# Optimization experiments

Measured on AMD Instinct MI355X. Metric: run time of the kernel, lower is better.

The kernel has to match this reference:

```python
import jax, jax.numpy as jnp
import numpy as np

SIZES = jnp.array([128.0, 256.0, 512.0], dtype=jnp.float32)
RATIOS = jnp.array([0.5, 1.0, 2.0], dtype=jnp.float32)
SCORE_THR = 0.05
IOU_THR = 0.7
MIN_SIZE = 16.0
MAX_PROP = 1000
PRE_NMS = 1000


def _base_anchors():
    # torchvision-style base anchors: (x1,y1,x2,y2) centered at origin, rounded
    h_r = jnp.sqrt(RATIOS)
    w_r = 1.0 / h_r
    ws = (w_r[:, None] * SIZES[None, :]).reshape(-1)  # (9,)
    hs = (h_r[:, None] * SIZES[None, :]).reshape(-1)
    return jnp.round(jnp.stack([-ws, -hs, ws, hs], axis=1) / 2.0)  # (9,4)


def _grid_anchors(img_h, img_w, fh, fw):
    # stride = image_size // feature_size; anchors ordered (y, x, anchor)
    sh, sw = img_h // fh, img_w // fw
    sx = jnp.arange(fw, dtype=jnp.float32) * sw
    sy = jnp.arange(fh, dtype=jnp.float32) * sh
    yy, xx = jnp.meshgrid(sy, sx, indexing='ij')
    xf = xx.reshape(-1)
    yf = yy.reshape(-1)
    shifts = jnp.stack([xf, yf, xf, yf], axis=1)  # (H*W, 4)
    return (shifts[:, None, :] + _base_anchors()[None, :, :]).reshape(-1, 4)  # (H*W*9, 4)


def _conv(x, w, b, pad):
    y = jax.lax.conv_general_dilated(x, w, (1, 1), pad,
                                     dimension_numbers=('NCHW', 'OIHW', 'NCHW'))
    return y + b[None, :, None, None]


def _bbox_adjust(anchors, deltas):
    # anchors, deltas: (..., 4); deltas = (dx, dy, dw, dh)
    aw = anchors[..., 2] - anchors[..., 0]
    ah = anchors[..., 3] - anchors[..., 1]
    cx = anchors[..., 0] + 0.5 * aw
    cy = anchors[..., 1] + 0.5 * ah
    ncx = deltas[..., 0] * aw + cx
    ncy = deltas[..., 1] * ah + cy
    nw = jnp.exp(deltas[..., 2]) * aw
    nh = jnp.exp(deltas[..., 3]) * ah
    return jnp.stack([ncx - 0.5 * nw, ncy - 0.5 * nh,
                      ncx + 0.5 * nw, ncy + 0.5 * nh], axis=-1)


def _pairwise_iou(b):
    area = (b[:, 2] - b[:, 0]) * (b[:, 3] - b[:, 1])
    lt = jnp.maximum(b[:, None, :2], b[None, :, :2])
    rb = jnp.minimum(b[:, None, 2:], b[None, :, 2:])
    wh = jnp.clip(rb - lt, 0.0)
    inter = wh[..., 0] * wh[..., 1]
    return inter / (area[:, None] + area[None, :] - inter + 1e-8)


def _per_image(boxes, scores, img_h, img_w):
    # clip to image, filter small / low-score, greedy NMS, pad to MAX_PROP
    x1 = jnp.clip(boxes[:, 0], 0.0, img_w)
    y1 = jnp.clip(boxes[:, 1], 0.0, img_h)
    x2 = jnp.clip(boxes[:, 2], 0.0, img_w)
    y2 = jnp.clip(boxes[:, 3], 0.0, img_h)
    b = jnp.stack([x1, y1, x2, y2], axis=1)
    valid = ((x2 - x1) >= MIN_SIZE) & ((y2 - y1) >= MIN_SIZE) & (scores > SCORE_THR)
    s = jnp.where(valid, scores, -1.0)
    topv, topi = jax.lax.top_k(s, PRE_NMS)
    tb = b[topi]  # (PRE_NMS, 4) sorted by score desc
    iou = _pairwise_iou(tb)
    idx = jnp.arange(PRE_NMS)

    def body(i, keep):
        sup = (iou[i] > IOU_THR) & keep[i] & (idx > i)
        return keep & ~sup

    keep = jax.lax.fori_loop(0, PRE_NMS, body, jnp.ones(PRE_NMS, dtype=bool))
    s2 = jnp.where(keep & (topv > 0.0), topv, -1.0)
    fv, fi = jax.lax.top_k(s2, MAX_PROP)
    return jnp.where((fv > 0.0)[:, None], tb[fi], 0.0)  # (MAX_PROP, 4)


def _forward(image_list, feature_map, conv_w, conv_b, cls_w, cls_b, bbox_w, bbox_b):
    N, C, H, W = feature_map.shape
    img_h, img_w = image_list.shape[2], image_list.shape[3]
    out = _conv(feature_map, conv_w, conv_b, 'SAME')  # (N, mid, H, W)
    # faithful to original: cls reshaped directly (no permute), bbox permuted
    cls = jax.nn.sigmoid(_conv(out, cls_w, cls_b, 'VALID')).reshape(N, -1, 2)
    bb = _conv(out, bbox_w, bbox_b, 'VALID').transpose(0, 2, 3, 1).reshape(N, -1, 4)
    anchors = _grid_anchors(img_h, img_w, H, W)  # (H*W*9, 4)
    dec = _bbox_adjust(anchors[None], bb)        # (N, M, 4)
    scores = cls[:, :, 1]                        # objectness
    fh, fw = float(img_h), float(img_w)
    fb = jax.vmap(lambda bx, sc: _per_image(bx, sc, fh, fw))(dec, scores)  # (N, MAX_PROP, 4)
    roi = fb.reshape(-1, 4)
    bidx = jnp.repeat(jnp.arange(N, dtype=roi.dtype), MAX_PROP)[:, None]
    return jnp.concatenate([roi, bidx], axis=1)  # (N*MAX_PROP, 5)


def setup_inputs() -> dict:
    key = jax.random.key(0)
    ks = jax.random.split(key, 6)
    image_list = jax.random.normal(ks[0], (8, 3, 800, 800), dtype=jnp.float32)
    feature_map = jax.random.normal(ks[1], (8, 512, 50, 50), dtype=jnp.float32)
    conv_w = 0.02 * jax.random.normal(ks[2], (256, 512, 3, 3), dtype=jnp.float32)
    conv_b = jnp.zeros((256,), dtype=jnp.float32)
    cls_w = 0.02 * jax.random.normal(ks[3], (18, 256, 1, 1), dtype=jnp.float32)
    cls_b = jnp.zeros((18,), dtype=jnp.float32)
    bbox_w = 0.01 * jax.random.normal(ks[4], (36, 256, 1, 1), dtype=jnp.float32)
    bbox_b = jnp.zeros((36,), dtype=jnp.float32)
    return {"image_list": image_list, "feature_map": feature_map,
            "conv_w": conv_w, "conv_b": conv_b, "cls_w": cls_w, "cls_b": cls_b,
            "bbox_w": bbox_w, "bbox_b": bbox_b}


def reference(image_list, feature_map, conv_w, conv_b, cls_w, cls_b, bbox_w, bbox_b):
    return _forward(image_list, feature_map, conv_w, conv_b, cls_w, cls_b, bbox_w, bbox_b)
```

## Files before the change

### kernel.cpp

```cpp
#include <hip/hip_runtime.h>
#include <cstdint>

#define N_IMG 8
#define CIN 512
#define COUT 256
#define FH 50
#define FW 50
#define SPAT 2500
#define NANCH 22500
#define KTOP 1000

__global__ __launch_bounds__(128) void k_conv3(const float* __restrict__ in,
                                               const float* __restrict__ w,
                                               const float* __restrict__ bias,
                                               float* __restrict__ out)
{
    __shared__ double ind[2][672];

    const int tile = blockIdx.x, ocg = blockIdx.y, n = blockIdx.z;
    const int ty = tile / 5, tx = tile % 5;
    const int y0 = ty * 5, x0 = tx * 10;
    const int t = threadIdx.x;
    const int oc_l = t & 63;
    const int g = t >> 6;
    const int base_lx = g * 5;
    const int oc0 = ocg * 64;

    int soff[6];
#pragma unroll
    for (int k = 0; k < 6; k++) {
        int idx = t + k * 128;
        soff[k] = -1;
        if (idx < 672) {
            int c = idx / 84, rem = idx - c * 84;
            int iy = rem / 12, ix = rem - iy * 12;
            int y = y0 - 1 + iy, x = x0 - 1 + ix;
            if ((unsigned)y < 50u && (unsigned)x < 50u)
                soff[k] = (n * CIN + c) * SPAT + y * FW + x;
        }
    }

    const float* wrow = w + (size_t)(oc0 + oc_l) * (CIN * 9);

    double acc[5][5];
#pragma unroll
    for (int i = 0; i < 5; i++)
#pragma unroll
        for (int j = 0; j < 5; j++) acc[i][j] = 0.0;

    float rin[6];
#pragma unroll
    for (int k = 0; k < 6; k++) rin[k] = (soff[k] >= 0) ? in[soff[k]] : 0.0f;
    float wnxt[9];
#pragma unroll
    for (int k = 0; k < 9; k++) wnxt[k] = wrow[k];

    for (int cc = 0; cc < 64; ++cc) {
        const int cur = cc & 1;
#pragma unroll
        for (int k = 0; k < 6; k++) {
            int idx = t + k * 128;
            if (idx < 672) ind[cur][idx] = (double)rin[k];
        }
        __syncthreads();

        if (cc < 63) {
            const int coff = (cc + 1) * (8 * SPAT);
#pragma unroll
            for (int k = 0; k < 6; k++)
                rin[k] = (soff[k] >= 0) ? in[soff[k] + coff] : 0.0f;
        }

#pragma unroll 1
        for (int c = 0; c < 8; c++) {
            double wd[9];
#pragma unroll
            for (int k = 0; k < 9; k++) wd[k] = (double)wnxt[k];
            const int nidx = cc * 8 + c + 1;
            if (nidx < 512) {
                const float* wp = wrow + nidx * 9;
#pragma unroll
                for (int k = 0; k < 9; k++) wnxt[k] = wp[k];
            }
#pragma unroll
            for (int r = 0; r < 7; r++) {
                double drow[7];
#pragma unroll
                for (int j = 0; j < 7; j++)
                    drow[j] = ind[cur][c * 84 + r * 12 + base_lx + j];
#pragma unroll
                for (int dy = 0; dy < 3; dy++) {
                    const int iy = r - dy;
                    if (iy >= 0 && iy < 5) {
#pragma unroll
                        for (int dx = 0; dx < 3; dx++) {
                            const double wdv = wd[dy * 3 + dx];
#pragma unroll
                            for (int ix = 0; ix < 5; ix++)
                                acc[iy][ix] = fma(wdv, drow[ix + dx], acc[iy][ix]);
                        }
                    }
                }
            }
        }
    }

    const double b = (double)bias[oc0 + oc_l];
#pragma unroll
    for (int iy = 0; iy < 5; iy++)
#pragma unroll
        for (int ix = 0; ix < 5; ix++) {
            int y = y0 + iy, x = x0 + base_lx + ix;
            out[(n * COUT + oc0 + oc_l) * SPAT + y * FW + x] = (float)(acc[iy][ix] + b);
        }
}

__global__ __launch_bounds__(256) void k_heads(const float* __restrict__ conv1,
                                               const float* __restrict__ cls_w,
                                               const float* __restrict__ cls_b,
                                               const float* __restrict__ bbox_w,
                                               const float* __restrict__ bbox_b,
                                               double* __restrict__ boxesd,
                                               double* __restrict__ scored)
{
    __shared__ float feat[25 * 257];
    __shared__ double outb[54 * 25];
    const int blk = blockIdx.x, n = blockIdx.y;
    const int pos0 = blk * 25;
    const int t = threadIdx.x;

    for (int idx = t; idx < 6400; idx += 256) {
        int c = idx / 25, p = idx - c * 25;
        feat[p * 257 + c] = conv1[(n * COUT + c) * SPAT + pos0 + p];
    }
    __syncthreads();

    for (int u = t; u < 1350; u += 256) {
        const int oc = u % 54, p = u / 54;
        const float* wp = (oc < 18) ? (cls_w + oc * COUT) : (bbox_w + (oc - 18) * COUT);
        double s = (double)((oc < 18) ? cls_b[oc] : bbox_b[oc - 18]);
        const float* fp = &feat[p * 257];
#pragma unroll 8
        for (int c = 0; c < COUT; c++) s = fma((double)wp[c], (double)fp[c], s);
        outb[oc * 25 + p] = s;
    }
    __syncthreads();

    if (t < 225) {
        const int p = t / 9, k = t - p * 9;
        const int pos = pos0 + p;
        const int y = pos / 50, x = pos - y * 50;
        const int ri = k / 3, si = k - ri * 3;
        const double ratio = (ri == 0) ? 0.5 : ((ri == 1) ? 1.0 : 2.0);
        const double size = (si == 0) ? 128.0 : ((si == 1) ? 256.0 : 512.0);
        const double hr = sqrt(ratio), wr = 1.0 / hr;
        const double wsz = wr * size, hsz = hr * size;
        const double bx0 = rint(-wsz * 0.5), by0 = rint(-hsz * 0.5);
        const double bx1 = rint(wsz * 0.5), by1 = rint(hsz * 0.5);
        const double sxf = (double)(x * 16), syf = (double)(y * 16);
        const double a0 = sxf + bx0, a1 = syf + by0, a2 = sxf + bx1, a3 = syf + by1;
        const double aw = a2 - a0, ah = a3 - a1;
        const double cx = a0 + 0.5 * aw, cy = a1 + 0.5 * ah;
        const double d0 = outb[(18 + k * 4 + 0) * 25 + p];
        const double d1 = outb[(18 + k * 4 + 1) * 25 + p];
        const double d2 = outb[(18 + k * 4 + 2) * 25 + p];
        const double d3 = outb[(18 + k * 4 + 3) * 25 + p];
        const double ncx = d0 * aw + cx, ncy = d1 * ah + cy;
        const double nw = exp(d2) * aw, nh = exp(d3) * ah;
        double x1 = ncx - 0.5 * nw, y1 = ncy - 0.5 * nh;
        double x2 = ncx + 0.5 * nw, y2 = ncy + 0.5 * nh;
        x1 = fmin(fmax(x1, 0.0), 800.0);
        y1 = fmin(fmax(y1, 0.0), 800.0);
        x2 = fmin(fmax(x2, 0.0), 800.0);
        y2 = fmin(fmax(y2, 0.0), 800.0);
        double* bp = boxesd + ((size_t)n * NANCH + pos * 9 + k) * 4;
        bp[0] = x1; bp[1] = y1; bp[2] = x2; bp[3] = y2;
    }
    for (int u = t; u < 450; u += 256) {
        const int ch = u / 25, p = u - ch * 25;
        const int pos = pos0 + p;
        if (pos & 1) {
            const int a = ch * 1250 + ((pos - 1) >> 1);
            const double v = outb[ch * 25 + p];
            scored[(size_t)n * NANCH + a] = 1.0 / (1.0 + exp(-v));
        }
    }
}

__global__ __launch_bounds__(1024) void k_select(const double* __restrict__ boxesd,
                                                 const double* __restrict__ scored,
                                                 uint64_t* __restrict__ keys,
                                                 double* __restrict__ tbd,
                                                 float* __restrict__ topv)
{
    __shared__ unsigned hist[256];
    __shared__ uint64_t selk[1024];
    __shared__ uint32_t seli[1024];
    __shared__ uint64_t sh_prefix, sh_mask;
    __shared__ unsigned sh_rem, sh_cntA, sh_cntB;

    const int n = blockIdx.x, t = threadIdx.x;
    uint64_t* ky = keys + (size_t)n * NANCH;

    for (int a = t; a < NANCH; a += 1024) {
        const double* bp = boxesd + ((size_t)n * NANCH + a) * 4;
        double x1 = bp[0], y1 = bp[1], x2 = bp[2], y2 = bp[3];
        double s0 = scored[(size_t)n * NANCH + a];
        bool valid = (x2 - x1 >= 16.0) && (y2 - y1 >= 16.0) && (s0 > 0.05);
        double s = valid ? s0 : -1.0;
        uint64_t b = (uint64_t)__double_as_longlong(s);
        uint64_t su = (b >> 63) ? ~b : (b | 0x8000000000000000ull);
        ky[a] = su;
    }
    if (t == 0) { sh_prefix = 0; sh_mask = 0; sh_rem = KTOP; }
    __syncthreads();

    for (int pass = 0; pass < 8; pass++) {
        const int shift = 56 - 8 * pass;
        if (t < 256) hist[t] = 0;
        __syncthreads();
        const uint64_t pre = sh_prefix, msk = sh_mask;
        for (int a = t; a < NANCH; a += 1024) {
            uint64_t k = ky[a];
            if ((k & msk) == pre)
                atomicAdd(&hist[(unsigned)((k >> shift) & 255)], 1u);
        }
        __syncthreads();
        if (t == 0) {
            unsigned rem = sh_rem;
            int v = 255;
            for (; v > 0; v--) {
                unsigned c = hist[v];
                if (rem <= c) break;
                rem -= c;
            }
            sh_prefix = pre | ((uint64_t)(unsigned)v << shift);
            sh_mask = msk | (255ull << shift);
            sh_rem = rem;
        }
        __syncthreads();
    }
    const uint64_t T = sh_prefix;
    selk[t] = 0; seli[t] = 0xFFFFFFFFu;
    if (t == 0) { sh_cntA = 0; sh_cntB = 0; }
    __syncthreads();
    for (int a = t; a < NANCH; a += 1024) {
        uint64_t k = ky[a];
        if (k > T) {
            unsigned p = atomicAdd(&sh_cntA, 1u);
            selk[p] = k; seli[p] = (uint32_t)a;
        }
    }
    __syncthreads();
    const unsigned m = sh_cntA;
    for (int a = t; a < NANCH; a += 1024) {
        uint64_t k = ky[a];
        if (k == T) {
            unsigned q = atomicAdd(&sh_cntB, 1u);
            unsigned slot = m + q;
            if (slot < KTOP) { selk[slot] = k; seli[slot] = (uint32_t)a; }
        }
    }
    __syncthreads();
    for (int k2 = 2; k2 <= 1024; k2 <<= 1) {
        for (int j = k2 >> 1; j > 0; j >>= 1) {
            int ixj = t ^ j;
            if (ixj > t) {
                bool asc = ((t & k2) == 0);
                uint64_t ka = selk[t], kb = selk[ixj];
                uint32_t ia = seli[t], ib = seli[ixj];
                bool gt = (ka > kb) || (ka == kb && ia < ib);
                if (gt == asc) { selk[t] = kb; selk[ixj] = ka; seli[t] = ib; seli[ixj] = ia; }
            }
            __syncthreads();
        }
    }
    if (t < KTOP) {
        uint64_t k = selk[1023 - t];
        uint32_t idx = seli[1023 - t];
        uint64_t b = (k >> 63) ? (k ^ 0x8000000000000000ull) : ~k;
        double s = __longlong_as_double((long long)b);
        const double* bp = boxesd + ((size_t)n * NANCH + idx) * 4;
        double* tp = tbd + ((size_t)n * KTOP + t) * 4;
        tp[0] = bp[0]; tp[1] = bp[1]; tp[2] = bp[2]; tp[3] = bp[3];
        topv[n * KTOP + t] = (float)s;
    }
}

__global__ __launch_bounds__(256) void k_supmat(const double* __restrict__ tbd,
                                                uint64_t* __restrict__ sup)
{
    __shared__ double sb[4000];
    const int tile = blockIdx.x, n = blockIdx.y;
    const int t = threadIdx.x;
    for (int i = t; i < 4000; i += 256) sb[i] = tbd[(size_t)n * KTOP * 4 + i];
    __syncthreads();
    const int r0 = tile * 64;
    for (int u = t; u < 1024; u += 256) {
        const int il = u >> 4, wq = u & 15;
        const int i = r0 + il;
        if (i >= 1000) continue;
        const double bix = sb[i * 4], biy = sb[i * 4 + 1], biz = sb[i * 4 + 2], biw = sb[i * 4 + 3];
        const double ai = (biz - bix) * (biw - biy);
        uint64_t bits = 0;
        const int jbase = wq * 64;
        for (int jj = 0; jj < 64; jj++) {
            const int j = jbase + jj;
            if (j < 1000 && j > i) {
                const double bjx = sb[j * 4], bjy = sb[j * 4 + 1], bjz = sb[j * 4 + 2], bjw = sb[j * 4 + 3];
                const double aj = (bjz - bjx) * (bjw - bjy);
                const double ltx = fmax(bix, bjx), lty = fmax(biy, bjy);
                const double rbx = fmin(biz, bjz), rby = fmin(biw, bjw);
                const double ww = fmax(rbx - ltx, 0.0), hh = fmax(rby - lty, 0.0);
                const double inter = ww * hh;
                const double iou = inter / (ai + aj - inter + 1e-8);
                if (iou > 0.7) bits |= (1ull << jj);
            }
        }
        sup[((size_t)n * KTOP + i) * 16 + wq] = bits;
    }
}

__global__ __launch_bounds__(64) void k_nms(const uint64_t* __restrict__ sup,
                                            uint64_t* __restrict__ keepout)
{
    const int n = blockIdx.x;
    const int lane = threadIdx.x;
    const uint64_t* rows = sup + (size_t)n * KTOP * 16;

    uint64_t keep;
    if (lane < 15) keep = ~0ull;
    else if (lane == 15) keep = (1ull << 40) - 1;
    else keep = 0;

    uint64_t A[8], B[8];
    auto LOADG = [&](uint64_t* dst, int g) {
#pragma unroll
        for (int k = 0; k < 8; k++) {
            int i = g * 8 + k;
            dst[k] = (lane < 16) ? rows[(size_t)i * 16 + lane] : 0ull;
        }
    };
    auto PROCG = [&](const uint64_t* src, int g) {
#pragma unroll
        for (int k = 0; k < 8; k++) {
            int i = g * 8 + k;
            uint64_t kw = __shfl(keep, i >> 6);
            bool alive = (kw >> (i & 63)) & 1ull;
            keep &= alive ? ~src[k] : ~0ull;
        }
    };

    LOADG(A, 0);
    for (int g = 0; g < 125; g += 2) {
        if (g + 1 < 125) LOADG(B, g + 1);
        PROCG(A, g);
        if (g + 2 < 125) LOADG(A, g + 2);
        if (g + 1 < 125) PROCG(B, g + 1);
    }
    if (lane < 16) keepout[n * 16 + lane] = keep;
}

__global__ __launch_bounds__(1024) void k_final(const uint64_t* __restrict__ keepw,
                                                const float* __restrict__ topv,
                                                const double* __restrict__ tbd,
                                                float* __restrict__ out)
{
    __shared__ int sc[1024];
    __shared__ uint64_t kw[16];
    __shared__ int sh_total;
    const int n = blockIdx.x, t = threadIdx.x;
    if (t < 16) kw[t] = keepw[n * 16 + t];
    __syncthreads();

    int val = 0;
    bool kept = false;
    if (t < 1000) {
        bool bit = (kw[t >> 6] >> (t & 63)) & 1ull;
        float v = topv[n * KTOP + t];
        kept = bit && (v > 0.0f);
        val = kept ? 1 : 0;
    }
    sc[t] = val;
    __syncthreads();
    for (int off = 1; off < 1024; off <<= 1) {
        int x = (t >= off) ? sc[t - off] : 0;
        __syncthreads();
        sc[t] += x;
        __syncthreads();
    }
    if (t == 1023) sh_total = sc[1023];
    __syncthreads();
    const int total = sh_total;
    if (t < 1000) {
        if (kept) {
            int r = sc[t] - 1;
            const double* bp = tbd + ((size_t)n * KTOP + t) * 4;
            float* o = out + ((size_t)n * KTOP + r) * 5;
            o[0] = (float)bp[0]; o[1] = (float)bp[1];
            o[2] = (float)bp[2]; o[3] = (float)bp[3];
            o[4] = (float)n;
        }
        if (t >= total) {
            float* o = out + ((size_t)n * KTOP + t) * 5;
            o[0] = 0.0f; o[1] = 0.0f; o[2] = 0.0f; o[3] = 0.0f; o[4] = (float)n;
        }
    }
}

extern "C" void kernel_launch(void* const* d_in, const int* in_sizes, int n_in,
                              void* d_out, int out_size, void* d_ws, size_t ws_size,
                              hipStream_t stream)
{
    (void)in_sizes; (void)n_in; (void)out_size; (void)ws_size;
    const float* feat   = (const float*)d_in[1];
    const float* conv_w = (const float*)d_in[2];
    const float* conv_b = (const float*)d_in[3];
    const float* cls_w  = (const float*)d_in[4];
    const float* cls_b  = (const float*)d_in[5];
    const float* bbox_w = (const float*)d_in[6];
    const float* bbox_b = (const float*)d_in[7];

    char* ws = (char*)d_ws;
    float*    conv1  = (float*)(ws);
    double*   boxesd = (double*)(ws + 20480000);
    double*   scored = (double*)(ws + 26240000);
    uint64_t* keys   = (uint64_t*)(ws + 27680000);
    double*   tbd    = (double*)(ws + 29120000);
    float*    topv   = (float*)(ws + 29376000);
    uint64_t* sup    = (uint64_t*)(ws + 29408000);
    uint64_t* keepw  = (uint64_t*)(ws + 30432000);
    float* out = (float*)d_out;

    k_conv3 <<<dim3(50, 4, 8), 128, 0, stream>>>(feat, conv_w, conv_b, conv1);
    k_heads <<<dim3(100, 8),   256, 0, stream>>>(conv1, cls_w, cls_b, bbox_w, bbox_b, boxesd, scored);
    k_select<<<8, 1024, 0, stream>>>(boxesd, scored, keys, tbd, topv);
    k_supmat<<<dim3(16, 8), 256, 0, stream>>>(tbd, sup);
    k_nms   <<<8, 64, 0, stream>>>(sup, keepw);
    k_final <<<8, 1024, 0, stream>>>(keepw, topv, tbd, out);
}
```

Before: 1.647 ms.

## Shrink conv3 tiles to 5x5 with 64-thread blocks and vectorized LDS reads

Each conv block now covers a 5x5 spatial tile with one wavefront of 64 threads instead of a 5x10 tile with two, which doubles the grid to 3200 blocks. The shared-memory input tile is repacked with an 8-wide padded row stride so each thread's 7-element row can be read as three double2 loads plus one scalar. The aim is more blocks for load balancing and occupancy, plus fewer LDS instructions in the FP64 inner loop. In exchange, halo overhead per output rises (7x7 loaded for 5x5 instead of 7x12 for 5x10), and each weight row is now fetched by twice as many blocks.

```diff
diff --git a/kernel.cpp b/kernel.cpp
--- a/kernel.cpp
+++ b/kernel.cpp
@@ -10,37 +10,36 @@
 #define NANCH 22500
 #define KTOP 1000
 
-__global__ __launch_bounds__(128) void k_conv3(const float* __restrict__ in,
-                                               const float* __restrict__ w,
-                                               const float* __restrict__ bias,
-                                               float* __restrict__ out)
-{
-    __shared__ double ind[2][672];
+__global__ __launch_bounds__(64) void k_conv3(const float* __restrict__ in,
+                                              const float* __restrict__ w,
+                                              const float* __restrict__ bias,
+                                              float* __restrict__ out)
+{
+    __shared__ double ind[2][8 * 7 * 8];
 
     const int tile = blockIdx.x, ocg = blockIdx.y, n = blockIdx.z;
-    const int ty = tile / 5, tx = tile % 5;
-    const int y0 = ty * 5, x0 = tx * 10;
+    const int ty = tile / 10, tx = tile % 10;
+    const int y0 = ty * 5, x0 = tx * 5;
     const int t = threadIdx.x;
-    const int oc_l = t & 63;
-    const int g = t >> 6;
-    const int base_lx = g * 5;
     const int oc0 = ocg * 64;
 
-    int soff[6];
-#pragma unroll
-    for (int k = 0; k < 6; k++) {
-        int idx = t + k * 128;
-        soff[k] = -1;
-        if (idx < 672) {
-            int c = idx / 84, rem = idx - c * 84;
-            int iy = rem / 12, ix = rem - iy * 12;
+    int soff[7];
+    int loff[7];
+#pragma unroll
+    for (int k = 0; k < 7; k++) {
+        int idx = t + k * 64;
+        soff[k] = -1; loff[k] = 0;
+        if (idx < 392) {
+            int c = idx / 49, rem = idx - c * 49;
+            int iy = rem / 7, ix = rem - iy * 7;
+            loff[k] = c * 56 + iy * 8 + ix;
             int y = y0 - 1 + iy, x = x0 - 1 + ix;
             if ((unsigned)y < 50u && (unsigned)x < 50u)
                 soff[k] = (n * CIN + c) * SPAT + y * FW + x;
         }
     }
 
-    const float* wrow = w + (size_t)(oc0 + oc_l) * (CIN * 9);
+    const float* wrow = w + (size_t)(oc0 + t) * (CIN * 9);
 
     double acc[5][5];
 #pragma unroll
@@ -48,9 +47,9 @@
 #pragma unroll
         for (int j = 0; j < 5; j++) acc[i][j] = 0.0;
 
-    float rin[6];
-#pragma unroll
-    for (int k = 0; k < 6; k++) rin[k] = (soff[k] >= 0) ? in[soff[k]] : 0.0f;
+    float rin[7];
+#pragma unroll
+    for (int k = 0; k < 7; k++) rin[k] = (soff[k] >= 0) ? in[soff[k]] : 0.0f;
     float wnxt[9];
 #pragma unroll
     for (int k = 0; k < 9; k++) wnxt[k] = wrow[k];
@@ -58,16 +57,16 @@
     for (int cc = 0; cc < 64; ++cc) {
         const int cur = cc & 1;
 #pragma unroll
-        for (int k = 0; k < 6; k++) {
-            int idx = t + k * 128;
-            if (idx < 672) ind[cur][idx] = (double)rin[k];
+        for (int k = 0; k < 7; k++) {
+            int idx = t + k * 64;
+            if (idx < 392) ind[cur][loff[k]] = (double)rin[k];
         }
         __syncthreads();
 
         if (cc < 63) {
             const int coff = (cc + 1) * (8 * SPAT);
 #pragma unroll
-            for (int k = 0; k < 6; k++)
+            for (int k = 0; k < 7; k++)
                 rin[k] = (soff[k] >= 0) ? in[soff[k] + coff] : 0.0f;
         }
 
@@ -84,10 +83,16 @@
             }
 #pragma unroll
             for (int r = 0; r < 7; r++) {
+                const double* rp = &ind[cur][c * 56 + r * 8];
                 double drow[7];
-#pragma unroll
-                for (int j = 0; j < 7; j++)
-                    drow[j] = ind[cur][c * 84 + r * 12 + base_lx + j];
+                {
+                    const double2* rp2 = reinterpret_cast<const double2*>(rp);
+                    double2 p0 = rp2[0], p1 = rp2[1], p2 = rp2[2];
+                    drow[0] = p0.x; drow[1] = p0.y;
+                    drow[2] = p1.x; drow[3] = p1.y;
+                    drow[4] = p2.x; drow[5] = p2.y;
+                    drow[6] = rp[6];
+                }
 #pragma unroll
                 for (int dy = 0; dy < 3; dy++) {
                     const int iy = r - dy;
@@ -105,13 +110,13 @@
         }
     }
 
-    const double b = (double)bias[oc0 + oc_l];
+    const double b = (double)bias[oc0 + t];
 #pragma unroll
     for (int iy = 0; iy < 5; iy++)
 #pragma unroll
         for (int ix = 0; ix < 5; ix++) {
-            int y = y0 + iy, x = x0 + base_lx + ix;
-            out[(n * COUT + oc0 + oc_l) * SPAT + y * FW + x] = (float)(acc[iy][ix] + b);
+            int y = y0 + iy, x = x0 + ix;
+            out[(n * COUT + oc0 + t) * SPAT + y * FW + x] = (float)(acc[iy][ix] + b);
         }
 }
 
@@ -432,7 +437,7 @@
     uint64_t* keepw  = (uint64_t*)(ws + 30432000);
     float* out = (float*)d_out;
 
-    k_conv3 <<<dim3(50, 4, 8), 128, 0, stream>>>(feat, conv_w, conv_b, conv1);
+    k_conv3 <<<dim3(100, 4, 8), 64, 0, stream>>>(feat, conv_w, conv_b, conv1);
     k_heads <<<dim3(100, 8),   256, 0, stream>>>(conv1, cls_w, cls_b, bbox_w, bbox_b, boxesd, scored);
     k_select<<<8, 1024, 0, stream>>>(boxesd, scored, keys, tbd, topv);
     k_supmat<<<dim3(16, 8), 256, 0, stream>>>(tbd, sup);
```

After: 1.704 ms. 3.5% more time.

## Split conv3x3 input-channel reduction in two halves with combine kernel

Applied to the files above, without the earlier changes.

Splits the 3x3 conv's 512-channel reduction across two block groups (split-K), doubling the grid from 1600 to 3200 blocks so the GPU is better filled. Each half writes fp64 partial sums to workspace, and a new combine kernel adds them with the bias into the fp32 conv output. This costs extra global traffic for the fp64 partials and one more launch. It also adds a trailing __syncthreads per iteration, and falls back to the old single-pass kernel when the workspace is too small.

```diff
diff --git a/kernel.cpp b/kernel.cpp
--- a/kernel.cpp
+++ b/kernel.cpp
@@ -9,15 +9,17 @@
 #define SPAT 2500
 #define NANCH 22500
 #define KTOP 1000
-
-__global__ __launch_bounds__(128) void k_conv3(const float* __restrict__ in,
-                                               const float* __restrict__ w,
-                                               const float* __restrict__ bias,
-                                               float* __restrict__ out)
+#define PART_ELEMS 5120000
+
+__global__ __launch_bounds__(128) void k_conv3_part(const float* __restrict__ in,
+                                                    const float* __restrict__ w,
+                                                    double* __restrict__ parts)
 {
     __shared__ double ind[2][672];
 
-    const int tile = blockIdx.x, ocg = blockIdx.y, n = blockIdx.z;
+    const int tile = blockIdx.x, ocg = blockIdx.y;
+    const int n = blockIdx.z >> 1, half = blockIdx.z & 1;
+    const int cc0 = half << 5, cc1 = cc0 + 32;
     const int ty = tile / 5, tx = tile % 5;
     const int y0 = ty * 5, x0 = tx * 10;
     const int t = threadIdx.x;
@@ -49,13 +51,19 @@
         for (int j = 0; j < 5; j++) acc[i][j] = 0.0;
 
     float rin[6];
-#pragma unroll
-    for (int k = 0; k < 6; k++) rin[k] = (soff[k] >= 0) ? in[soff[k]] : 0.0f;
+    {
+        const int coff0 = cc0 * (8 * SPAT);
+#pragma unroll
+        for (int k = 0; k < 6; k++) rin[k] = (soff[k] >= 0) ? in[soff[k] + coff0] : 0.0f;
+    }
     float wnxt[9];
-#pragma unroll
-    for (int k = 0; k < 9; k++) wnxt[k] = wrow[k];
-
-    for (int cc = 0; cc < 64; ++cc) {
+    {
+        const float* wp0 = wrow + cc0 * 72;
+#pragma unroll
+        for (int k = 0; k < 9; k++) wnxt[k] = wp0[k];
+    }
+
+    for (int cc = cc0; cc < cc1; ++cc) {
         const int cur = cc & 1;
 #pragma unroll
         for (int k = 0; k < 6; k++) {
@@ -64,7 +72,7 @@
         }
         __syncthreads();
 
-        if (cc < 63) {
+        if (cc + 1 < cc1) {
             const int coff = (cc + 1) * (8 * SPAT);
 #pragma unroll
             for (int k = 0; k < 6; k++)
@@ -77,7 +85,7 @@
 #pragma unroll
             for (int k = 0; k < 9; k++) wd[k] = (double)wnxt[k];
             const int nidx = cc * 8 + c + 1;
-            if (nidx < 512) {
+            if (nidx < cc1 * 8) {
                 const float* wp = wrow + nidx * 9;
 #pragma unroll
                 for (int k = 0; k < 9; k++) wnxt[k] = wp[k];
@@ -103,6 +111,120 @@
                 }
             }
         }
+        __syncthreads();
+    }
+
+    double* po = parts + (size_t)half * PART_ELEMS + (size_t)(n * COUT + oc0 + oc_l) * SPAT;
+#pragma unroll
+    for (int iy = 0; iy < 5; iy++)
+#pragma unroll
+        for (int ix = 0; ix < 5; ix++)
+            po[(y0 + iy) * FW + (x0 + base_lx + ix)] = acc[iy][ix];
+}
+
+__global__ __launch_bounds__(256) void k_combine(const double* __restrict__ parts,
+                                                 const float* __restrict__ bias,
+                                                 float* __restrict__ out)
+{
+    const int i = blockIdx.x * 256 + threadIdx.x;
+    if (i < PART_ELEMS) {
+        const int oc = (i / SPAT) & 255;
+        out[i] = (float)(parts[i] + parts[i + PART_ELEMS] + (double)bias[oc]);
+    }
+}
+
+__global__ __launch_bounds__(128) void k_conv3_full(const float* __restrict__ in,
+                                                    const float* __restrict__ w,
+                                                    const float* __restrict__ bias,
+                                                    float* __restrict__ out)
+{
+    __shared__ double ind[2][672];
+
+    const int tile = blockIdx.x, ocg = blockIdx.y, n = blockIdx.z;
+    const int ty = tile / 5, tx = tile % 5;
+    const int y0 = ty * 5, x0 = tx * 10;
+    const int t = threadIdx.x;
+    const int oc_l = t & 63;
+    const int g = t >> 6;
+    const int base_lx = g * 5;
+    const int oc0 = ocg * 64;
+
+    int soff[6];
+#pragma unroll
+    for (int k = 0; k < 6; k++) {
+        int idx = t + k * 128;
+        soff[k] = -1;
+        if (idx < 672) {
+            int c = idx / 84, rem = idx - c * 84;
+            int iy = rem / 12, ix = rem - iy * 12;
+            int y = y0 - 1 + iy, x = x0 - 1 + ix;
+            if ((unsigned)y < 50u && (unsigned)x < 50u)
+                soff[k] = (n * CIN + c) * SPAT + y * FW + x;
+        }
+    }
+
+    const float* wrow = w + (size_t)(oc0 + oc_l) * (CIN * 9);
+
+    double acc[5][5];
+#pragma unroll
+    for (int i = 0; i < 5; i++)
+#pragma unroll
+        for (int j = 0; j < 5; j++) acc[i][j] = 0.0;
+
+    float rin[6];
+#pragma unroll
+    for (int k = 0; k < 6; k++) rin[k] = (soff[k] >= 0) ? in[soff[k]] : 0.0f;
+    float wnxt[9];
+#pragma unroll
+    for (int k = 0; k < 9; k++) wnxt[k] = wrow[k];
+
+    for (int cc = 0; cc < 64; ++cc) {
+        const int cur = cc & 1;
+#pragma unroll
+        for (int k = 0; k < 6; k++) {
+            int idx = t + k * 128;
+            if (idx < 672) ind[cur][idx] = (double)rin[k];
+        }
+        __syncthreads();
+        if (cc < 63) {
+            const int coff = (cc + 1) * (8 * SPAT);
+#pragma unroll
+            for (int k = 0; k < 6; k++)
+                rin[k] = (soff[k] >= 0) ? in[soff[k] + coff] : 0.0f;
+        }
+#pragma unroll 1
+        for (int c = 0; c < 8; c++) {
+            double wd[9];
+#pragma unroll
+            for (int k = 0; k < 9; k++) wd[k] = (double)wnxt[k];
+            const int nidx = cc * 8 + c + 1;
+            if (nidx < 512) {
+                const float* wp = wrow + nidx * 9;
+#pragma unroll
+                for (int k = 0; k < 9; k++) wnxt[k] = wp[k];
+            }
+#pragma unroll
+            for (int r = 0; r < 7; r++) {
+                double drow[7];
+#pragma unroll
+                for (int j = 0; j < 7; j++)
+                    drow[j] = ind[cur][c * 84 + r * 12 + base_lx + j];
+#pragma unroll
+                for (int dy = 0; dy < 3; dy++) {
+                    const int iy = r - dy;
+                    if (iy >= 0 && iy < 5) {
+#pragma unroll
+                        for (int dx = 0; dx < 3; dx++) {
+                            const double wdv = wd[dy * 3 + dx];
+#pragma unroll
+                            for (int ix = 0; ix < 5; ix++)
+                                acc[iy][ix] = fma(wdv, drow[ix + dx], acc[iy][ix]);
+                        }
+                    }
+                }
+            }
+        }
+        __syncthreads();
     }
 
     const double b = (double)bias[oc0 + oc_l];
@@ -412,7 +534,7 @@
                               void* d_out, int out_size, void* d_ws, size_t ws_size,
                               hipStream_t stream)
 {
-    (void)in_sizes; (void)n_in; (void)out_size; (void)ws_size;
+    (void)in_sizes; (void)n_in; (void)out_size;
     const float* feat   = (const float*)d_in[1];
     const float* conv_w = (const float*)d_in[2];
     const float* conv_b = (const float*)d_in[3];
@@ -420,22 +542,45 @@
     const float* cls_b  = (const float*)d_in[5];
     const float* bbox_w = (const float*)d_in[6];
     const float* bbox_b = (const float*)d_in[7];
-
+    float* out = (float*)d_out;
     char* ws = (char*)d_ws;
-    float*    conv1  = (float*)(ws);
-    double*   boxesd = (double*)(ws + 20480000);
-    double*   scored = (double*)(ws + 26240000);
-    uint64_t* keys   = (uint64_t*)(ws + 27680000);
-    double*   tbd    = (double*)(ws + 29120000);
-    float*    topv   = (float*)(ws + 29376000);
-    uint64_t* sup    = (uint64_t*)(ws + 29408000);
-    uint64_t* keepw  = (uint64_t*)(ws + 30432000);
-    float* out = (float*)d_out;
-
-    k_conv3 <<<dim3(50, 4, 8), 128, 0, stream>>>(feat, conv_w, conv_b, conv1);
-    k_heads <<<dim3(100, 8),   256, 0, stream>>>(conv1, cls_w, cls_b, bbox_w, bbox_b, boxesd, scored);
-    k_select<<<8, 1024, 0, stream>>>(boxesd, scored, keys, tbd, topv);
-    k_supmat<<<dim3(16, 8), 256, 0, stream>>>(tbd, sup);
-    k_nms   <<<8, 64, 0, stream>>>(sup, keepw);
-    k_final <<<8, 1024, 0, stream>>>(keepw, topv, tbd, out);
-}
+
+    const size_t NEED_SPLIT = 2ull * 40960000 + 20480000 + 5760000 + 1440000
+                            + 1440000 + 256000 + 32000 + 1024000 + 1024;
+
+    if (ws_size >= NEED_SPLIT) {
+        double*   parts  = (double*)(ws);
+        float*    conv1  = (float*)(ws + 81920000);
+        double*   boxesd = (double*)(ws + 102400000);
+        double*   scored = (double*)(ws + 108160000);
+        uint64_t* keys   = (uint64_t*)(ws + 109600000);
+        double*   tbd    = (double*)(ws + 111040000);
+        float*    topv   = (float*)(ws + 111296000);
+        uint64_t* sup    = (uint64_t*)(ws + 111328000);
+        uint64_t* keepw  = (uint64_t*)(ws + 112352000);
+
+        k_conv3_part<<<dim3(50, 4, 16), 128, 0, stream>>>(feat, conv_w, parts);
+        k_combine   <<<(PART_ELEMS + 255) / 256, 256, 0, stream>>>(parts, conv_b, conv1);
+        k_heads <<<dim3(100, 8),   256, 0, stream>>>(conv1, cls_w, cls_b, bbox_w, bbox_b, boxesd, scored);
+        k_select<<<8, 1024, 0, stream>>>(boxesd, scored, keys, tbd, topv);
+        k_supmat<<<dim3(16, 8), 256, 0, stream>>>(tbd, sup);
+        k_nms   <<<8, 64, 0, stream>>>(sup, keepw);
+        k_final <<<8, 1024, 0, stream>>>(keepw, topv, tbd, out);
+    } else {
+        float*    conv1  = (float*)(ws);
+        double*   boxesd = (double*)(ws + 20480000);
+        double*   scored = (double*)(ws + 26240000);
+        uint64_t* keys   = (uint64_t*)(ws + 27680000);
+        double*   tbd    = (double*)(ws + 29120000);
+        float*    topv   = (float*)(ws + 29376000);
+        uint64_t* sup    = (uint64_t*)(ws + 29408000);
+        uint64_t* keepw  = (uint64_t*)(ws + 30432000);
+
+        k_conv3_full<<<dim3(50, 4, 8), 128, 0, stream>>>(feat, conv_w, conv_b, conv1);
+        k_heads <<<dim3(100, 8),   256, 0, stream>>>(conv1, cls_w, cls_b, bbox_w, bbox_b, boxesd, scored);
+        k_select<<<8, 1024, 0, stream>>>(boxesd, scored, keys, tbd, topv);
+        k_supmat<<<dim3(16, 8), 256, 0, stream>>>(tbd, sup);
+        k_nms   <<<8, 64, 0, stream>>>(sup, keepw);
+        k_final <<<8, 1024, 0, stream>>>(keepw, topv, tbd, out);
+    }
+}
```

After: 1.583 ms. 1.04x faster.
